# Kernel optimization log

Measured on AMD Instinct MI355X. Metric: run time of the kernel, lower is better.

Reference implementation:

```python
import jax, jax.numpy as jnp
import numpy as np

B, H, N, D = 2, 16, 2048, 128

def setup_inputs() -> dict:
    key = jax.random.key(0)
    kq, kk, kv = jax.random.split(key, 3)
    q = jax.random.normal(kq, (B, H, N, D), dtype=jnp.float32)
    k = jax.random.normal(kk, (B, H, N, D), dtype=jnp.float32)
    v = jax.random.normal(kv, (B, H, N, D), dtype=jnp.float32)
    return {"q": q, "k": k, "v": v}

def reference(q, k, v):
    # scale = 1/sqrt(d) computed at forward time (scale=None in __init__)
    d = q.shape[-1]
    scale = 1.0 / jnp.sqrt(jnp.asarray(d, dtype=q.dtype))
    # scores: (B, H, N, N)
    scores = jnp.einsum('bhnd,bhmd->bhnm', q, k) * scale
    probs = jax.nn.softmax(scores, axis=-1)
    return jnp.einsum('bhnm,bhmd->bhnd', probs, v)
```

## Files before the change

kernel.cpp:

```cpp
#include <hip/hip_runtime.h>
#include <hip/hip_fp16.h>

#define BH   32
#define SEQ  2048
#define DIM  128
#define CK   32
#define NCH  (SEQ / CK)
#define CSZ  (CK * DIM)

typedef _Float16 half8   __attribute__((ext_vector_type(8)));
typedef __fp16   fp16x2  __attribute__((ext_vector_type(2)));
typedef _Float16 half2v  __attribute__((ext_vector_type(2)));
typedef float    floatx4 __attribute__((ext_vector_type(4)));

__device__ inline half2v pk2(float a, float b) {
    fp16x2 t = __builtin_amdgcn_cvt_pkrtz(a, b);
    return *(half2v*)&t;
}
__device__ inline half8 pk8(float4 a, float4 b) {
    half2v l0 = pk2(a.x, a.y), l1 = pk2(a.z, a.w);
    half2v l2 = pk2(b.x, b.y), l3 = pk2(b.z, b.w);
    half8 h;
    h[0] = l0[0]; h[1] = l0[1]; h[2] = l1[0]; h[3] = l1[1];
    h[4] = l2[0]; h[5] = l2[1]; h[6] = l3[0]; h[7] = l3[1];
    return h;
}

__device__ inline void ld16(const void* g, void* l) {
    __builtin_amdgcn_global_load_lds(
        (__attribute__((address_space(1))) void*)(uintptr_t)g,
        (__attribute__((address_space(3))) void*)(uintptr_t)l, 16, 0, 0);
}

#define SYNC_VML do {                                              \
    asm volatile("s_waitcnt vmcnt(0) lgkmcnt(0)" ::: "memory");    \
    __builtin_amdgcn_s_barrier();                                  \
    asm volatile("" ::: "memory");                                 \
} while (0)

__global__ void prep_kernel(const float* __restrict__ k, const float* __restrict__ v,
                            _Float16* __restrict__ kh, _Float16* __restrict__ vt) {
    const float SC = 0.08838834764831845f * 1.4426950408889634f;
    __shared__ __align__(16) _Float16 t[32][136];
    const int bh = blockIdx.x >> 6;
    const int kc = blockIdx.x & 63;
    const int tid = threadIdx.x;
    const size_t base = ((size_t)bh * SEQ + kc * CK) * DIM;

    const float4* kf4 = (const float4*)(k + base);
    const float4* vf4 = (const float4*)(v + base);
    half8* kh8 = (half8*)(kh + base);

    #pragma unroll
    for (int i = 0; i < 2; i++) {
        int f8 = i * 256 + tid;
        float4 a = kf4[2 * f8], b = kf4[2 * f8 + 1];
        a.x *= SC; a.y *= SC; a.z *= SC; a.w *= SC;
        b.x *= SC; b.y *= SC; b.z *= SC; b.w *= SC;
        kh8[f8] = pk8(a, b);
        int row = f8 >> 4, c8 = f8 & 15;
        *((half8*)&t[row][c8 * 8]) = pk8(vf4[2 * f8], vf4[2 * f8 + 1]);
    }
    __syncthreads();
    _Float16* vout = vt + ((size_t)bh * NCH + kc) * (DIM * CK);
    #pragma unroll
    for (int i = 0; i < 2; i++) {
        int g = i * 256 + tid;
        int d = g >> 2, kg = g & 3;
        half8 h;
        #pragma unroll
        for (int j = 0; j < 8; j++) h[j] = t[kg * 8 + j][d];
        *((half8*)(vout + d * CK + kg * 8)) = h;
    }
}

__global__ __launch_bounds__(128, 2) void attn_kernel(
        const float* __restrict__ q, const _Float16* __restrict__ kh,
        const _Float16* __restrict__ vt, float* __restrict__ out) {
    __shared__ __align__(16) _Float16 Kbuf[2][CSZ];
    __shared__ __align__(16) _Float16 Vbuf[2][CSZ];

    const int lid = blockIdx.x + (blockIdx.y << 5);
    const int xcd = lid & 7;
    const int idx = lid >> 3;
    const int bh  = (xcd << 2) + (idx >> 5);
    const int qt  = idx & 31;

    const int tid  = threadIdx.x;
    const int w    = tid >> 6;
    const int lane = tid & 63;
    const int l15  = lane & 15;
    const int quad = lane >> 4;

    half8 qf[2][4];
    #pragma unroll
    for (int s = 0; s < 2; s++) {
        const float* qb = q + ((size_t)bh * SEQ + qt * 64 + w * 32 + s * 16 + l15) * DIM;
        #pragma unroll
        for (int c = 0; c < 4; c++) {
            float4 a = *((const float4*)(qb + c * 32 + quad * 8));
            float4 b = *((const float4*)(qb + c * 32 + quad * 8 + 4));
            qf[s][c] = pk8(a, b);
        }
    }

    half8 ones;
    #pragma unroll
    for (int j = 0; j < 8; j++) ones[j] = (_Float16)1.0f;

    floatx4 zf = {0.f, 0.f, 0.f, 0.f};
    floatx4 O[2][8];
    #pragma unroll
    for (int s = 0; s < 2; s++)
        #pragma unroll
        for (int i = 0; i < 8; i++) O[s][i] = zf;
    floatx4 Osum[2] = {zf, zf};

    const _Float16* kb = kh + (size_t)bh * SEQ * DIM;
    const _Float16* vb = vt + (size_t)bh * SEQ * DIM;

    const _Float16* kgp[4];
    const _Float16* vgp[4];
    #pragma unroll
    for (int i = 0; i < 4; i++) {
        int si = w * 256 + i * 64 + lane;
        int rho = si >> 4, Pos = si & 15;
        int g = (Pos - 3 * rho) & 15;
        int key = (((rho >> 2) & 3) << 3) + ((rho >> 4) << 2) + (rho & 3);
        kgp[i] = kb + key * DIM + g * 8;
        int vo = ((si >> 6) * 16 + (si & 15)) * CK + ((si >> 4) & 3) * 8;
        vgp[i] = vb + vo;
    }

    auto dma = [&](int kc, int b_) {
        size_t off = (size_t)kc * CSZ;
        #pragma unroll
        for (int i = 0; i < 4; i++) {
            ld16(kgp[i] + off, &Kbuf[b_][(w * 4 + i) * 512]);
            ld16(vgp[i] + off, &Vbuf[b_][(w * 4 + i) * 512]);
        }
    };

    half8 pf0, pf1;
    half8 vfr[8];
    #pragma unroll
    for (int j = 0; j < 8; j++) { pf0[j] = (_Float16)0.0f; pf1[j] = (_Float16)0.0f; }
    #pragma unroll
    for (int dt = 0; dt < 8; dt++)
        #pragma unroll
        for (int j = 0; j < 8; j++) vfr[dt][j] = (_Float16)0.0f;

    auto body = [&](int b_) {
        const _Float16* Kc = Kbuf[b_];
        const _Float16* Vc = Vbuf[b_];

        floatx4 S[2][2];
        #pragma unroll
        for (int s = 0; s < 2; s++) { S[s][0] = zf; S[s][1] = zf; }
        __builtin_amdgcn_s_setprio(1);
        #pragma unroll
        for (int c = 0; c < 4; c++) {
            #pragma unroll
            for (int j = 0; j < 2; j++) {
                int rho = j * 16 + l15;
                int Pos = (c * 4 + quad + 3 * rho) & 15;
                half8 ka = *((const half8*)&Kc[rho * DIM + Pos * 8]);
                S[0][j] = __builtin_amdgcn_mfma_f32_16x16x32_f16(ka, qf[0][c], S[0][j], 0, 0, 0);
                S[1][j] = __builtin_amdgcn_mfma_f32_16x16x32_f16(ka, qf[1][c], S[1][j], 0, 0, 0);
            }
        }
        __builtin_amdgcn_s_setprio(0);

        half8 vn[8];
        #pragma unroll
        for (int dt = 0; dt < 8; dt++)
            vn[dt] = *((const half8*)&Vc[dt * 512 + (quad * 16 + l15) * 8]);

        half8 pn0, pn1;
        {
            float4 a, b;
            a.x = __builtin_amdgcn_exp2f(S[0][0][0]);
            a.y = __builtin_amdgcn_exp2f(S[0][0][1]);
            a.z = __builtin_amdgcn_exp2f(S[0][0][2]);
            a.w = __builtin_amdgcn_exp2f(S[0][0][3]);
            b.x = __builtin_amdgcn_exp2f(S[0][1][0]);
            b.y = __builtin_amdgcn_exp2f(S[0][1][1]);
            b.z = __builtin_amdgcn_exp2f(S[0][1][2]);
            b.w = __builtin_amdgcn_exp2f(S[0][1][3]);
            pn0 = pk8(a, b);
            a.x = __builtin_amdgcn_exp2f(S[1][0][0]);
            a.y = __builtin_amdgcn_exp2f(S[1][0][1]);
            a.z = __builtin_amdgcn_exp2f(S[1][0][2]);
            a.w = __builtin_amdgcn_exp2f(S[1][0][3]);
            b.x = __builtin_amdgcn_exp2f(S[1][1][0]);
            b.y = __builtin_amdgcn_exp2f(S[1][1][1]);
            b.z = __builtin_amdgcn_exp2f(S[1][1][2]);
            b.w = __builtin_amdgcn_exp2f(S[1][1][3]);
            pn1 = pk8(a, b);
        }

        __builtin_amdgcn_s_setprio(1);
        Osum[0] = __builtin_amdgcn_mfma_f32_16x16x32_f16(pf0, ones, Osum[0], 0, 0, 0);
        Osum[1] = __builtin_amdgcn_mfma_f32_16x16x32_f16(pf1, ones, Osum[1], 0, 0, 0);
        #pragma unroll
        for (int dt = 0; dt < 8; dt++) {
            O[0][dt] = __builtin_amdgcn_mfma_f32_16x16x32_f16(pf0, vfr[dt], O[0][dt], 0, 0, 0);
            O[1][dt] = __builtin_amdgcn_mfma_f32_16x16x32_f16(pf1, vfr[dt], O[1][dt], 0, 0, 0);
        }
        __builtin_amdgcn_s_setprio(0);

        #pragma unroll
        for (int dt = 0; dt < 8; dt++) vfr[dt] = vn[dt];
        pf0 = pn0; pf1 = pn1;
    };

    dma(0, 0);

    #pragma unroll 2
    for (int kc = 0; kc < NCH; kc++) {
        SYNC_VML;
        if (kc + 1 < NCH) dma(kc + 1, (kc + 1) & 1);
        body(kc & 1);
    }

    __builtin_amdgcn_s_setprio(1);
    Osum[0] = __builtin_amdgcn_mfma_f32_16x16x32_f16(pf0, ones, Osum[0], 0, 0, 0);
    Osum[1] = __builtin_amdgcn_mfma_f32_16x16x32_f16(pf1, ones, Osum[1], 0, 0, 0);
    #pragma unroll
    for (int dt = 0; dt < 8; dt++) {
        O[0][dt] = __builtin_amdgcn_mfma_f32_16x16x32_f16(pf0, vfr[dt], O[0][dt], 0, 0, 0);
        O[1][dt] = __builtin_amdgcn_mfma_f32_16x16x32_f16(pf1, vfr[dt], O[1][dt], 0, 0, 0);
    }
    __builtin_amdgcn_s_setprio(0);

    #pragma unroll
    for (int s = 0; s < 2; s++) {
        float* ob = out + ((size_t)bh * SEQ + qt * 64 + w * 32 + s * 16) * DIM;
        #pragma unroll
        for (int r = 0; r < 4; r++) {
            float rinv = 1.0f / Osum[s][r];
            #pragma unroll
            for (int dt = 0; dt < 8; dt++) {
                ob[(size_t)(quad * 4 + r) * DIM + dt * 16 + l15] = O[s][dt][r] * rinv;
            }
        }
    }
}

extern "C" void kernel_launch(void* const* d_in, const int* in_sizes, int n_in,
                              void* d_out, int out_size, void* d_ws, size_t ws_size,
                              hipStream_t stream) {
    const float* q = (const float*)d_in[0];
    const float* k = (const float*)d_in[1];
    const float* v = (const float*)d_in[2];
    float* out = (float*)d_out;

    const size_t elems = (size_t)BH * SEQ * DIM;
    _Float16* kh = (_Float16*)d_ws;
    _Float16* vtp = kh + elems;

    prep_kernel<<<BH * NCH, 256, 0, stream>>>(k, v, kh, vtp);
    attn_kernel<<<dim3(SEQ / 64, BH), 128, 0, stream>>>(q, kh, vtp, out);
}
```

Measured before the change: 201.8 us.

## Switch attention to 32x32x16 MFMA with 128-query tiles and XOR-swizzled LDS

Replaces the 16x16x32 MFMA tiling with 32x32x16 MFMA, so each wave handles 32 query rows with a single 32x32 score accumulator. Blocks grow to 256 threads covering 128 queries, which halves how often each K/V chunk is loaded per query. LDS layouts for K and V change to an XOR swizzle to avoid bank conflicts. The P fragment for the PV product is rebuilt with cross-half lane shuffles. The costs are extra shuffle and select work per chunk, V-fragment loads no longer overlapped through a separate prefetch register set, and fewer blocks in flight.

```diff
diff --git a/kernel.cpp b/kernel.cpp
--- a/kernel.cpp
+++ b/kernel.cpp
@@ -12,10 +12,15 @@
 typedef __fp16   fp16x2  __attribute__((ext_vector_type(2)));
 typedef _Float16 half2v  __attribute__((ext_vector_type(2)));
 typedef float    floatx4 __attribute__((ext_vector_type(4)));
+typedef float    floatx16 __attribute__((ext_vector_type(16)));
 
 __device__ inline half2v pk2(float a, float b) {
     fp16x2 t = __builtin_amdgcn_cvt_pkrtz(a, b);
     return *(half2v*)&t;
+}
+__device__ inline unsigned pk2u(float a, float b) {
+    fp16x2 t = __builtin_amdgcn_cvt_pkrtz(a, b);
+    return *(unsigned*)&t;
 }
 __device__ inline half8 pk8(float4 a, float4 b) {
     half2v l0 = pk2(a.x, a.y), l1 = pk2(a.z, a.w);
@@ -74,33 +79,32 @@
     }
 }
 
-__global__ __launch_bounds__(128, 2) void attn_kernel(
+__global__ __launch_bounds__(256, 2) void attn_kernel(
         const float* __restrict__ q, const _Float16* __restrict__ kh,
         const _Float16* __restrict__ vt, float* __restrict__ out) {
     __shared__ __align__(16) _Float16 Kbuf[2][CSZ];
     __shared__ __align__(16) _Float16 Vbuf[2][CSZ];
 
-    const int lid = blockIdx.x + (blockIdx.y << 5);
+    const int lid = blockIdx.x + (blockIdx.y << 4);
     const int xcd = lid & 7;
     const int idx = lid >> 3;
-    const int bh  = (xcd << 2) + (idx >> 5);
-    const int qt  = idx & 31;
+    const int bh  = (xcd << 2) + (idx >> 4);
+    const int qt  = idx & 15;
 
     const int tid  = threadIdx.x;
     const int w    = tid >> 6;
     const int lane = tid & 63;
-    const int l15  = lane & 15;
-    const int quad = lane >> 4;
-
-    half8 qf[2][4];
-    #pragma unroll
-    for (int s = 0; s < 2; s++) {
-        const float* qb = q + ((size_t)bh * SEQ + qt * 64 + w * 32 + s * 16 + l15) * DIM;
-        #pragma unroll
-        for (int c = 0; c < 4; c++) {
-            float4 a = *((const float4*)(qb + c * 32 + quad * 8));
-            float4 b = *((const float4*)(qb + c * 32 + quad * 8 + 4));
-            qf[s][c] = pk8(a, b);
+    const int l31  = lane & 31;
+    const int hi   = lane >> 5;
+
+    half8 qf[8];
+    {
+        const float* qb = q + ((size_t)bh * SEQ + qt * 128 + w * 32 + l31) * DIM + hi * 8;
+        #pragma unroll
+        for (int ki = 0; ki < 8; ki++) {
+            float4 a = *((const float4*)(qb + ki * 16));
+            float4 b = *((const float4*)(qb + ki * 16 + 4));
+            qf[ki] = pk8(a, b);
         }
     }
 
@@ -108,110 +112,95 @@
     #pragma unroll
     for (int j = 0; j < 8; j++) ones[j] = (_Float16)1.0f;
 
-    floatx4 zf = {0.f, 0.f, 0.f, 0.f};
-    floatx4 O[2][8];
-    #pragma unroll
-    for (int s = 0; s < 2; s++)
-        #pragma unroll
-        for (int i = 0; i < 8; i++) O[s][i] = zf;
-    floatx4 Osum[2] = {zf, zf};
+    floatx16 zf16;
+    #pragma unroll
+    for (int i = 0; i < 16; i++) zf16[i] = 0.f;
+
+    floatx16 O[4];
+    #pragma unroll
+    for (int dtv = 0; dtv < 4; dtv++) O[dtv] = zf16;
+    floatx16 Osum = zf16;
 
     const _Float16* kb = kh + (size_t)bh * SEQ * DIM;
     const _Float16* vb = vt + (size_t)bh * SEQ * DIM;
 
-    const _Float16* kgp[4];
-    const _Float16* vgp[4];
-    #pragma unroll
-    for (int i = 0; i < 4; i++) {
-        int si = w * 256 + i * 64 + lane;
-        int rho = si >> 4, Pos = si & 15;
-        int g = (Pos - 3 * rho) & 15;
-        int key = (((rho >> 2) & 3) << 3) + ((rho >> 4) << 2) + (rho & 3);
-        kgp[i] = kb + key * DIM + g * 8;
-        int vo = ((si >> 6) * 16 + (si & 15)) * CK + ((si >> 4) & 3) * 8;
-        vgp[i] = vb + vo;
-    }
+    const int sk0 = tid, sk1 = tid + 256;
+    const _Float16* kgp0 = kb + (sk0 >> 4) * DIM + (((sk0 & 15) ^ ((sk0 >> 4) & 7)) * 8);
+    const _Float16* kgp1 = kb + (sk1 >> 4) * DIM + (((sk1 & 15) ^ ((sk1 >> 4) & 7)) * 8);
+    const _Float16* vgp0 = vb + (sk0 >> 2) * CK + (((sk0 & 3) ^ ((sk0 >> 2) & 3)) * 8);
+    const _Float16* vgp1 = vb + (sk1 >> 2) * CK + (((sk1 & 3) ^ ((sk1 >> 2) & 3)) * 8);
 
     auto dma = [&](int kc, int b_) {
         size_t off = (size_t)kc * CSZ;
-        #pragma unroll
-        for (int i = 0; i < 4; i++) {
-            ld16(kgp[i] + off, &Kbuf[b_][(w * 4 + i) * 512]);
-            ld16(vgp[i] + off, &Vbuf[b_][(w * 4 + i) * 512]);
-        }
+        ld16(kgp0 + off, &Kbuf[b_][w * 512]);
+        ld16(kgp1 + off, &Kbuf[b_][2048 + w * 512]);
+        ld16(vgp0 + off, &Vbuf[b_][w * 512]);
+        ld16(vgp1 + off, &Vbuf[b_][2048 + w * 512]);
     };
 
-    half8 pf0, pf1;
-    half8 vfr[8];
-    #pragma unroll
-    for (int j = 0; j < 8; j++) { pf0[j] = (_Float16)0.0f; pf1[j] = (_Float16)0.0f; }
-    #pragma unroll
-    for (int dt = 0; dt < 8; dt++)
-        #pragma unroll
-        for (int j = 0; j < 8; j++) vfr[dt][j] = (_Float16)0.0f;
+    half8 pf[2];
+    half8 vfr[4][2];
+    #pragma unroll
+    for (int i = 0; i < 2; i++)
+        #pragma unroll
+        for (int j = 0; j < 8; j++) pf[i][j] = (_Float16)0.0f;
+    #pragma unroll
+    for (int dtv = 0; dtv < 4; dtv++)
+        #pragma unroll
+        for (int ks = 0; ks < 2; ks++)
+            #pragma unroll
+            for (int j = 0; j < 8; j++) vfr[dtv][ks][j] = (_Float16)0.0f;
 
     auto body = [&](int b_) {
         const _Float16* Kc = Kbuf[b_];
         const _Float16* Vc = Vbuf[b_];
 
-        floatx4 S[2][2];
-        #pragma unroll
-        for (int s = 0; s < 2; s++) { S[s][0] = zf; S[s][1] = zf; }
+        floatx16 S = zf16;
         __builtin_amdgcn_s_setprio(1);
         #pragma unroll
-        for (int c = 0; c < 4; c++) {
+        for (int ki = 0; ki < 8; ki++) {
+            half8 kf = *((const half8*)&Kc[l31 * DIM + (((ki * 2 + hi) ^ (l31 & 7)) * 8)]);
+            S = __builtin_amdgcn_mfma_f32_32x32x16_f16(kf, qf[ki], S, 0, 0, 0);
+        }
+        __builtin_amdgcn_s_setprio(0);
+
+        __builtin_amdgcn_s_setprio(1);
+        Osum = __builtin_amdgcn_mfma_f32_32x32x16_f16(pf[0], ones, Osum, 0, 0, 0);
+        Osum = __builtin_amdgcn_mfma_f32_32x32x16_f16(pf[1], ones, Osum, 0, 0, 0);
+        #pragma unroll
+        for (int dtv = 0; dtv < 4; dtv++) {
+            O[dtv] = __builtin_amdgcn_mfma_f32_32x32x16_f16(pf[0], vfr[dtv][0], O[dtv], 0, 0, 0);
+            O[dtv] = __builtin_amdgcn_mfma_f32_32x32x16_f16(pf[1], vfr[dtv][1], O[dtv], 0, 0, 0);
+        }
+        __builtin_amdgcn_s_setprio(0);
+
+        #pragma unroll
+        for (int dtv = 0; dtv < 4; dtv++)
             #pragma unroll
-            for (int j = 0; j < 2; j++) {
-                int rho = j * 16 + l15;
-                int Pos = (c * 4 + quad + 3 * rho) & 15;
-                half8 ka = *((const half8*)&Kc[rho * DIM + Pos * 8]);
-                S[0][j] = __builtin_amdgcn_mfma_f32_16x16x32_f16(ka, qf[0][c], S[0][j], 0, 0, 0);
-                S[1][j] = __builtin_amdgcn_mfma_f32_16x16x32_f16(ka, qf[1][c], S[1][j], 0, 0, 0);
-            }
-        }
-        __builtin_amdgcn_s_setprio(0);
-
-        half8 vn[8];
-        #pragma unroll
-        for (int dt = 0; dt < 8; dt++)
-            vn[dt] = *((const half8*)&Vc[dt * 512 + (quad * 16 + l15) * 8]);
-
-        half8 pn0, pn1;
-        {
-            float4 a, b;
-            a.x = __builtin_amdgcn_exp2f(S[0][0][0]);
-            a.y = __builtin_amdgcn_exp2f(S[0][0][1]);
-            a.z = __builtin_amdgcn_exp2f(S[0][0][2]);
-            a.w = __builtin_amdgcn_exp2f(S[0][0][3]);
-            b.x = __builtin_amdgcn_exp2f(S[0][1][0]);
-            b.y = __builtin_amdgcn_exp2f(S[0][1][1]);
-            b.z = __builtin_amdgcn_exp2f(S[0][1][2]);
-            b.w = __builtin_amdgcn_exp2f(S[0][1][3]);
-            pn0 = pk8(a, b);
-            a.x = __builtin_amdgcn_exp2f(S[1][0][0]);
-            a.y = __builtin_amdgcn_exp2f(S[1][0][1]);
-            a.z = __builtin_amdgcn_exp2f(S[1][0][2]);
-            a.w = __builtin_amdgcn_exp2f(S[1][0][3]);
-            b.x = __builtin_amdgcn_exp2f(S[1][1][0]);
-            b.y = __builtin_amdgcn_exp2f(S[1][1][1]);
-            b.z = __builtin_amdgcn_exp2f(S[1][1][2]);
-            b.w = __builtin_amdgcn_exp2f(S[1][1][3]);
-            pn1 = pk8(a, b);
-        }
-
-        __builtin_amdgcn_s_setprio(1);
-        Osum[0] = __builtin_amdgcn_mfma_f32_16x16x32_f16(pf0, ones, Osum[0], 0, 0, 0);
-        Osum[1] = __builtin_amdgcn_mfma_f32_16x16x32_f16(pf1, ones, Osum[1], 0, 0, 0);
-        #pragma unroll
-        for (int dt = 0; dt < 8; dt++) {
-            O[0][dt] = __builtin_amdgcn_mfma_f32_16x16x32_f16(pf0, vfr[dt], O[0][dt], 0, 0, 0);
-            O[1][dt] = __builtin_amdgcn_mfma_f32_16x16x32_f16(pf1, vfr[dt], O[1][dt], 0, 0, 0);
-        }
-        __builtin_amdgcn_s_setprio(0);
-
-        #pragma unroll
-        for (int dt = 0; dt < 8; dt++) vfr[dt] = vn[dt];
-        pf0 = pn0; pf1 = pn1;
+            for (int ks = 0; ks < 2; ks++)
+                vfr[dtv][ks] = *((const half8*)&Vc[(dtv * 32 + l31) * CK +
+                                                   (((ks * 2 + hi) ^ (lane & 3)) * 8)]);
+
+        unsigned wv[8], xv[8];
+        #pragma unroll
+        for (int i = 0; i < 8; i++) {
+            float e0 = __builtin_amdgcn_exp2f(S[2 * i]);
+            float e1 = __builtin_amdgcn_exp2f(S[2 * i + 1]);
+            wv[i] = pk2u(e0, e1);
+        }
+        #pragma unroll
+        for (int i = 0; i < 8; i++) xv[i] = __shfl_xor((int)wv[i], 32);
+        union { unsigned u[4]; half8 h; } c0, c1;
+        c0.u[0] = hi ? xv[2] : wv[0];
+        c0.u[1] = hi ? xv[3] : wv[1];
+        c0.u[2] = hi ? wv[2] : xv[0];
+        c0.u[3] = hi ? wv[3] : xv[1];
+        c1.u[0] = hi ? xv[6] : wv[4];
+        c1.u[1] = hi ? xv[7] : wv[5];
+        c1.u[2] = hi ? wv[6] : xv[4];
+        c1.u[3] = hi ? wv[7] : xv[5];
+        pf[0] = c0.h;
+        pf[1] = c1.h;
     };
 
     dma(0, 0);
@@ -224,24 +213,24 @@
     }
 
     __builtin_amdgcn_s_setprio(1);
-    Osum[0] = __builtin_amdgcn_mfma_f32_16x16x32_f16(pf0, ones, Osum[0], 0, 0, 0);
-    Osum[1] = __builtin_amdgcn_mfma_f32_16x16x32_f16(pf1, ones, Osum[1], 0, 0, 0);
-    #pragma unroll
-    for (int dt = 0; dt < 8; dt++) {
-        O[0][dt] = __builtin_amdgcn_mfma_f32_16x16x32_f16(pf0, vfr[dt], O[0][dt], 0, 0, 0);
-        O[1][dt] = __builtin_amdgcn_mfma_f32_16x16x32_f16(pf1, vfr[dt], O[1][dt], 0, 0, 0);
+    Osum = __builtin_amdgcn_mfma_f32_32x32x16_f16(pf[0], ones, Osum, 0, 0, 0);
+    Osum = __builtin_amdgcn_mfma_f32_32x32x16_f16(pf[1], ones, Osum, 0, 0, 0);
+    #pragma unroll
+    for (int dtv = 0; dtv < 4; dtv++) {
+        O[dtv] = __builtin_amdgcn_mfma_f32_32x32x16_f16(pf[0], vfr[dtv][0], O[dtv], 0, 0, 0);
+        O[dtv] = __builtin_amdgcn_mfma_f32_32x32x16_f16(pf[1], vfr[dtv][1], O[dtv], 0, 0, 0);
     }
     __builtin_amdgcn_s_setprio(0);
 
-    #pragma unroll
-    for (int s = 0; s < 2; s++) {
-        float* ob = out + ((size_t)bh * SEQ + qt * 64 + w * 32 + s * 16) * DIM;
-        #pragma unroll
-        for (int r = 0; r < 4; r++) {
-            float rinv = 1.0f / Osum[s][r];
+    {
+        float* ob = out + ((size_t)bh * SEQ + qt * 128 + w * 32) * DIM;
+        #pragma unroll
+        for (int r = 0; r < 16; r++) {
+            int qrow = (r & 3) + 8 * (r >> 2) + 4 * hi;
+            float rinv = 1.0f / Osum[r];
             #pragma unroll
-            for (int dt = 0; dt < 8; dt++) {
-                ob[(size_t)(quad * 4 + r) * DIM + dt * 16 + l15] = O[s][dt][r] * rinv;
+            for (int dtv = 0; dtv < 4; dtv++) {
+                ob[(size_t)qrow * DIM + dtv * 32 + l31] = O[dtv][r] * rinv;
             }
         }
     }
@@ -260,5 +249,5 @@
     _Float16* vtp = kh + elems;
 
     prep_kernel<<<BH * NCH, 256, 0, stream>>>(k, v, kh, vtp);
-    attn_kernel<<<dim3(SEQ / 64, BH), 128, 0, stream>>>(q, kh, vtp, out);
-}
+    attn_kernel<<<dim3(SEQ / 128, BH), 256, 0, stream>>>(q, kh, vtp, out);
+}
```

Measured after the change: 219.6 us. 1.09x slower.
